# Optimization experiments

Measured on AMD Instinct MI355X. Metric: run time of the kernel, lower is better.

Reference implementation:

```python
import jax, jax.numpy as jnp
import numpy as np


def setup_inputs() -> dict:
    key = jax.random.key(0)
    k1, k2 = jax.random.split(key)
    K, D = 512, 64
    x = jax.random.normal(k1, (64, D, 32, 32), dtype=jnp.float32)
    # torch init: uniform(-1/k, 1/k)
    weight = jax.random.uniform(k2, (D, K), dtype=jnp.float32, minval=-1.0 / K, maxval=1.0 / K)
    return {"x": x, "weight": weight}


def reference(x, weight):
    # x: [B, d, *spatial]; weight: [d, k]
    B, d = x.shape[0], x.shape[1]
    spatial = x.shape[2:]
    xf = x.reshape(B, d, -1)                      # [B, d, N]
    x2 = jnp.sum(xf * xf, axis=1)                 # [B, N]
    w2 = jnp.sum(weight * weight, axis=0)         # [k]
    dots = jnp.einsum('bdn,dk->bnk', xf, weight)  # [B, N, k]
    dist = x2[..., None] - 2.0 * dots + w2        # [B, N, k]
    argmin = jnp.argmin(dist, axis=-1)            # [B, N]
    quantized = jnp.take(weight.T, argmin, axis=0)          # [B, N, d]
    quantized = jnp.moveaxis(quantized.reshape(B, *spatial, d), -1, 1)  # [B, d, *spatial]
    return quantized, argmin.reshape(B, *spatial)
```

## Files before the change

### kernel.cpp

```cpp
#include <hip/hip_runtime.h>

#define KCODES 512
#define DDIM   64
#define NPIX   1024
#define QELEMS (64 * DDIM * NPIX)
#define PXB    64
#define FLAG_GAP 4e-5f

typedef float f32x4 __attribute__((ext_vector_type(4)));
typedef short bf16x8 __attribute__((ext_vector_type(8)));
typedef unsigned int u32;
typedef u32 u32x4 __attribute__((ext_vector_type(4)));


__device__ __forceinline__ bf16x8 pack_hi(const float* f) {
  u32x4 wds;
#pragma unroll
  for (int p = 0; p < 4; ++p) {
    u32 u0 = __float_as_uint(f[2 * p]);
    u32 u1 = __float_as_uint(f[2 * p + 1]);
    wds[p] = (u0 >> 16) | (u1 & 0xffff0000u);
  }
  return __builtin_bit_cast(bf16x8, wds);
}
__device__ __forceinline__ bf16x8 pack_lo(const float* f) {
  u32x4 wds;
#pragma unroll
  for (int p = 0; p < 4; ++p) {
    float r0 = f[2 * p]     - __uint_as_float(__float_as_uint(f[2 * p])     & 0xffff0000u);
    float r1 = f[2 * p + 1] - __uint_as_float(__float_as_uint(f[2 * p + 1]) & 0xffff0000u);
    wds[p] = (__float_as_uint(r0) >> 16) | (__float_as_uint(r1) & 0xffff0000u);
  }
  return __builtin_bit_cast(bf16x8, wds);
}

__global__ void vq_prep(const float* __restrict__ w,
                        float* __restrict__ w2f_g,
                        bf16x8* __restrict__ frag) {
#pragma clang fp contract(off)
  const int blk = blockIdx.x;
  if (blk == 32) {
    int k = threadIdx.x;
    if (k < KCODES) {
      float s = 0.0f;
      for (int d = 0; d < DDIM; ++d) {
        float v = w[d * KCODES + k];
        float p = v * v;
        s = s + p;
      }
      w2f_g[k] = s;
    }
    return;
  }
  if (threadIdx.x >= 256) return;
  const int cg   = blk;
  const int t    = threadIdx.x >> 6;
  const int lane = threadIdx.x & 63;
  const int code = cg * 16 + (lane & 15);
  const int h    = t & 1;
  float f[8];
#pragma unroll
  for (int j = 0; j < 8; ++j)
    f[j] = w[(h * 32 + (lane >> 4) * 8 + j) * KCODES + code];
  frag[(cg * 4 + t) * 64 + lane] = (t < 2) ? pack_hi(f) : pack_lo(f);
}

__global__ __launch_bounds__(256) void vq_kernel(
    const float* __restrict__ x, const float* __restrict__ w,
    const float* __restrict__ w2f_g, const bf16x8* __restrict__ frag,
    float* __restrict__ qout, float* __restrict__ aout) {
#pragma clang fp contract(off)

  __shared__ float  xs[DDIM][PXB + 1];
  __shared__ float  w2fs[KCODES];
  __shared__ float  hm1[2][PXB], hm2[2][PXB];
  __shared__ int    hi1[2][PXB];
  __shared__ int    skm[PXB];

  const int tid  = threadIdx.x;
  const int lane = tid & 63;
  const int lr   = lane & 15;
  const int lg   = lane >> 4;
  const int wid  = __builtin_amdgcn_readfirstlane(tid >> 6);
  const int ch   = wid & 1;
  const int pgh  = wid >> 1;
  const int b    = blockIdx.x >> 4;
  const int n0   = (blockIdx.x & 15) * PXB;
  const size_t pixbase = (size_t)blockIdx.x * PXB;
  const int px0  = pgh * 32;

  {
    const float* xp = x + (size_t)b * (DDIM * NPIX) + n0;
#pragma unroll
    for (int dd = 0; dd < 16; ++dd) {
      int d = dd * 4 + wid;
      xs[d][lane] = xp[(size_t)d * NPIX + lane];
    }
  }
  w2fs[tid]       = w2f_g[tid];
  w2fs[tid + 256] = w2f_g[tid + 256];
  __syncthreads();

  bf16x8 bxh[2][2], bxl[2][2];
#pragma unroll
  for (int pg = 0; pg < 2; ++pg) {
#pragma unroll
    for (int h = 0; h < 2; ++h) {
      float f[8];
#pragma unroll
      for (int j = 0; j < 8; ++j)
        f[j] = xs[h * 32 + lg * 8 + j][px0 + pg * 16 + lr];
      bxh[pg][h] = pack_hi(f);
      bxl[pg][h] = pack_lo(f);
    }
  }

  float m1[2] = {3.4e38f, 3.4e38f};
  float m2[2] = {3.4e38f, 3.4e38f};
  int   i1[2] = {0, 0};
#pragma unroll 2
  for (int i = 0; i < 16; ++i) {
    const int cg = ch * 16 + i;
    const bf16x8* fr = frag + (size_t)cg * 256 + lane;
    bf16x8 awh0 = fr[0];
    bf16x8 awh1 = fr[64];
    bf16x8 awl0 = fr[128];
    bf16x8 awl1 = fr[192];

#pragma unroll
    for (int pg = 0; pg < 2; ++pg) {
      f32x4 acc = {0.f, 0.f, 0.f, 0.f};
      acc = __builtin_amdgcn_mfma_f32_16x16x32_bf16(awh0, bxh[pg][0], acc, 0, 0, 0);
      acc = __builtin_amdgcn_mfma_f32_16x16x32_bf16(awh1, bxh[pg][1], acc, 0, 0, 0);
      acc = __builtin_amdgcn_mfma_f32_16x16x32_bf16(awl0, bxh[pg][0], acc, 0, 0, 0);
      acc = __builtin_amdgcn_mfma_f32_16x16x32_bf16(awl1, bxh[pg][1], acc, 0, 0, 0);
      acc = __builtin_amdgcn_mfma_f32_16x16x32_bf16(awh0, bxl[pg][0], acc, 0, 0, 0);
      acc = __builtin_amdgcn_mfma_f32_16x16x32_bf16(awh1, bxl[pg][1], acc, 0, 0, 0);
      acc = __builtin_amdgcn_mfma_f32_16x16x32_bf16(awl0, bxl[pg][0], acc, 0, 0, 0);
      acc = __builtin_amdgcn_mfma_f32_16x16x32_bf16(awl1, bxl[pg][1], acc, 0, 0, 0);
      const int codebase = cg * 16 + lg * 4;
#pragma unroll
      for (int r = 0; r < 4; ++r) {
        int code = codebase + r;
        float s = fmaf(-2.0f, acc[r], w2fs[code]);
        float om = m1[pg];
        m1[pg] = fminf(om, s);
        m2[pg] = fminf(m2[pg], fmaxf(om, s));
        i1[pg] = (s < om) ? code : i1[pg];
      }
    }
  }

#pragma unroll
  for (int pg = 0; pg < 2; ++pg) {
#pragma unroll
    for (int mi = 0; mi < 2; ++mi) {
      int mask = mi ? 32 : 16;
      float pm1 = __shfl_xor(m1[pg], mask);
      float pm2 = __shfl_xor(m2[pg], mask);
      int   pi1 = __shfl_xor(i1[pg], mask);
      if (pm1 < m1[pg]) { m2[pg] = fminf(m1[pg], pm2); m1[pg] = pm1; i1[pg] = pi1; }
      else              { m2[pg] = fminf(m2[pg], pm1); }
    }
    if (lg == 0) {
      int px = px0 + pg * 16 + lr;
      hm1[ch][px] = m1[pg];
      hm2[ch][px] = m2[pg];
      hi1[ch][px] = i1[pg];
    }
  }
  __syncthreads();

  bool flg = false;
  if (lane < 32) {
    const int px = px0 + lane;
    float a1 = hm1[0][px], a2 = hm2[0][px];
    int   ai = hi1[0][px];
    float b1 = hm1[1][px], b2 = hm2[1][px];
    int   bi = hi1[1][px];
    float M1, M2;
    int   I1;
    if (b1 < a1) { M1 = b1; M2 = fminf(a1, b2); I1 = bi; }
    else         { M1 = a1; M2 = fminf(a2, b1); I1 = ai; }
    if (ch == 0) skm[px] = I1;
    flg = (M2 - M1 < FLAG_GAP);
  }
  unsigned long long bal = __ballot(flg);
  unsigned int fmask = (unsigned int)(bal & 0xFFFFFFFFu);

  {
    int idx = 0;
    while (fmask) {
      const int Lr = __builtin_ctz(fmask);
      fmask &= fmask - 1;
      if ((idx++ & 1) != ch) continue;
      const int L = px0 + Lr;
      float x2L = 0.0f;
      for (int d = 0; d < DDIM; ++d) {
        float xv = xs[d][L];
        float p = xv * xv;
        x2L = x2L + p;
      }
      const int k0 = lane * 8;
      float dots[8];
#pragma unroll
      for (int c = 0; c < 8; ++c) dots[c] = 0.f;
      for (int d = 0; d < DDIM; d += 4) {
        f32x4 wa[4][2];
        float xv[4];
#pragma unroll
        for (int u = 0; u < 4; ++u) {
          const float* wr = w + (size_t)(d + u) * KCODES + k0;
          wa[u][0] = *reinterpret_cast<const f32x4*>(wr);
          wa[u][1] = *reinterpret_cast<const f32x4*>(wr + 4);
          xv[u] = xs[d + u][L];
        }
#pragma unroll
        for (int u = 0; u < 4; ++u) {
#pragma unroll
          for (int c = 0; c < 4; ++c) {
            float p = xv[u] * wa[u][0][c];
            dots[c] = dots[c] + p;
          }
#pragma unroll
          for (int c = 0; c < 4; ++c) {
            float p = xv[u] * wa[u][1][c];
            dots[c + 4] = dots[c + 4] + p;
          }
        }
      }
      float bv = 3.4e38f;
      int   bi = 0;
#pragma unroll
      for (int c = 0; c < 8; ++c) {
        float t  = x2L - 2.0f * dots[c];
        float s2 = t + w2fs[k0 + c];
        if (s2 < bv) { bv = s2; bi = k0 + c; }
      }
#pragma unroll
      for (int off = 1; off < 64; off <<= 1) {
        float ov = __shfl_xor(bv, off);
        int   oi = __shfl_xor(bi, off);
        if (ov < bv || (ov == bv && oi < bi)) { bv = ov; bi = oi; }
      }
      if (lane == 0) skm[L] = bi;
    }
  }
  __syncthreads();

  if (tid < PXB) aout[pixbase + tid] = (float)skm[tid];

  {
    float* qp = qout + (size_t)b * (DDIM * NPIX) + n0;
#pragma unroll
    for (int i = 0; i < 16; ++i) {
      int d  = (tid >> 6) + i * 4;
      int px = tid & 63;
      qp[(size_t)d * NPIX + px] = w[d * KCODES + skm[px]];
    }
  }
}

extern "C" void kernel_launch(void* const* d_in, const int* in_sizes, int n_in,
                              void* d_out, int out_size, void* d_ws, size_t ws_size,
                              hipStream_t stream) {
  const float* x = (const float*)d_in[0];
  const float* w = (const float*)d_in[1];
  float* qout = (float*)d_out;
  float* aout = (float*)d_out + QELEMS;

  char*   wsb   = (char*)d_ws;
  float*  w2f_g = (float*)wsb;
  bf16x8* frag  = (bf16x8*)(wsb + 4096);

  vq_prep<<<33, 512, 0, stream>>>(w, w2f_g, frag);
  vq_kernel<<<(65536 / PXB), 256, 0, stream>>>(x, w, w2f_g, frag, qout, aout);
}
```

Before: 42.90 us.

## Halve pixels per block and split codebook four ways across waves

Each block now handles 32 pixels instead of 64. All four waves share the same pixels and each scans a quarter of the codebook, rather than two pixel groups times two codebook halves. This doubles the grid to 2048 blocks for better occupancy and balance. The merge now combines four partial top-2 results and rechecks flagged near-ties across four waves. In exchange, the x tile loads and output stores get narrower (32 floats per row), and each codebook fragment is reused across fewer pixels.

```diff
diff --git a/kernel.cpp b/kernel.cpp
--- a/kernel.cpp
+++ b/kernel.cpp
@@ -4,7 +4,7 @@
 #define DDIM   64
 #define NPIX   1024
 #define QELEMS (64 * DDIM * NPIX)
-#define PXB    64
+#define PXB    32
 #define FLAG_GAP 4e-5f
 
 typedef float f32x4 __attribute__((ext_vector_type(4)));
@@ -73,28 +73,27 @@
 
   __shared__ float  xs[DDIM][PXB + 1];
   __shared__ float  w2fs[KCODES];
-  __shared__ float  hm1[2][PXB], hm2[2][PXB];
-  __shared__ int    hi1[2][PXB];
+  __shared__ float  sm1[4][PXB], sm2[4][PXB];
+  __shared__ int    si1[4][PXB];
   __shared__ int    skm[PXB];
+  __shared__ unsigned long long s_fmask;
 
   const int tid  = threadIdx.x;
   const int lane = tid & 63;
   const int lr   = lane & 15;
   const int lg   = lane >> 4;
   const int wid  = __builtin_amdgcn_readfirstlane(tid >> 6);
-  const int ch   = wid & 1;
-  const int pgh  = wid >> 1;
-  const int b    = blockIdx.x >> 4;
-  const int n0   = (blockIdx.x & 15) * PXB;
+  const int b    = blockIdx.x >> 5;
+  const int n0   = (blockIdx.x & 31) * PXB;
   const size_t pixbase = (size_t)blockIdx.x * PXB;
-  const int px0  = pgh * 32;
 
   {
     const float* xp = x + (size_t)b * (DDIM * NPIX) + n0;
 #pragma unroll
-    for (int dd = 0; dd < 16; ++dd) {
-      int d = dd * 4 + wid;
-      xs[d][lane] = xp[(size_t)d * NPIX + lane];
+    for (int i = 0; i < 8; ++i) {
+      int d  = (tid >> 5) + i * 8;
+      int px = tid & 31;
+      xs[d][px] = xp[(size_t)d * NPIX + px];
     }
   }
   w2fs[tid]       = w2f_g[tid];
@@ -109,7 +108,7 @@
       float f[8];
 #pragma unroll
       for (int j = 0; j < 8; ++j)
-        f[j] = xs[h * 32 + lg * 8 + j][px0 + pg * 16 + lr];
+        f[j] = xs[h * 32 + lg * 8 + j][pg * 16 + lr];
       bxh[pg][h] = pack_hi(f);
       bxl[pg][h] = pack_lo(f);
     }
@@ -119,8 +118,8 @@
   float m2[2] = {3.4e38f, 3.4e38f};
   int   i1[2] = {0, 0};
 #pragma unroll 2
-  for (int i = 0; i < 16; ++i) {
-    const int cg = ch * 16 + i;
+  for (int i = 0; i < 8; ++i) {
+    const int cg = wid * 8 + i;
     const bf16x8* fr = frag + (size_t)cg * 256 + lane;
     bf16x8 awh0 = fr[0];
     bf16x8 awh1 = fr[64];
@@ -163,38 +162,36 @@
       else              { m2[pg] = fminf(m2[pg], pm1); }
     }
     if (lg == 0) {
-      int px = px0 + pg * 16 + lr;
-      hm1[ch][px] = m1[pg];
-      hm2[ch][px] = m2[pg];
-      hi1[ch][px] = i1[pg];
-    }
-  }
-  __syncthreads();
-
-  bool flg = false;
-  if (lane < 32) {
-    const int px = px0 + lane;
-    float a1 = hm1[0][px], a2 = hm2[0][px];
-    int   ai = hi1[0][px];
-    float b1 = hm1[1][px], b2 = hm2[1][px];
-    int   bi = hi1[1][px];
-    float M1, M2;
-    int   I1;
-    if (b1 < a1) { M1 = b1; M2 = fminf(a1, b2); I1 = bi; }
-    else         { M1 = a1; M2 = fminf(a2, b1); I1 = ai; }
-    if (ch == 0) skm[px] = I1;
-    flg = (M2 - M1 < FLAG_GAP);
-  }
-  unsigned long long bal = __ballot(flg);
-  unsigned int fmask = (unsigned int)(bal & 0xFFFFFFFFu);
+      int px = pg * 16 + lr;
+      sm1[wid][px] = m1[pg];
+      sm2[wid][px] = m2[pg];
+      si1[wid][px] = i1[pg];
+    }
+  }
+  __syncthreads();
+
+  if (tid < PXB) {
+    float M1 = sm1[0][tid], M2 = sm2[0][tid];
+    int   I1 = si1[0][tid];
+#pragma unroll
+    for (int c = 1; c < 4; ++c) {
+      float c1 = sm1[c][tid];
+      if (c1 < M1) { M2 = fminf(M1, sm2[c][tid]); M1 = c1; I1 = si1[c][tid]; }
+      else         { M2 = fminf(M2, c1); }
+    }
+    skm[tid] = I1;
+    unsigned long long bal = __ballot(M2 - M1 < FLAG_GAP);
+    if (tid == 0) s_fmask = bal;
+  }
+  __syncthreads();
 
   {
+    unsigned long long fm = s_fmask;
     int idx = 0;
-    while (fmask) {
-      const int Lr = __builtin_ctz(fmask);
-      fmask &= fmask - 1;
-      if ((idx++ & 1) != ch) continue;
-      const int L = px0 + Lr;
+    while (fm) {
+      const int L = __builtin_ctzll(fm);
+      fm &= (fm - 1);
+      if ((idx++ & 3) != wid) continue;
       float x2L = 0.0f;
       for (int d = 0; d < DDIM; ++d) {
         float xv = xs[d][L];
@@ -253,9 +250,9 @@
   {
     float* qp = qout + (size_t)b * (DDIM * NPIX) + n0;
 #pragma unroll
-    for (int i = 0; i < 16; ++i) {
-      int d  = (tid >> 6) + i * 4;
-      int px = tid & 63;
+    for (int i = 0; i < 8; ++i) {
+      int d  = (tid >> 5) + i * 8;
+      int px = tid & 31;
       qp[(size_t)d * NPIX + px] = w[d * KCODES + skm[px]];
     }
   }
```

Result: no change. 43.68 us (+1.8%).
